# Kernel optimization log

Hardware: AMD Instinct MI355X
Metric: run time of the kernel (lower is better)

## Reference

```python
import jax, jax.numpy as jnp
import numpy as np
import math

D = 256   # d_model / hidden_size
Q = 256   # q_num (query-side nodes)
K = 512   # k_num (key-side nodes)
NEG = -9e15


def _forward(q_enc, k_enc, rel_k, rel_v, k_adj,
             W_glob, b_glob, W_gv0, b_gv0, W_gv1, b_gv1,
             W_gq, b_gq, W_lq, b_lq,
             W_locgate, b_locgate, W_gate, b_gate):
    d = q_enc.shape[-1]
    scale = 1.0 / math.sqrt(d)
    act = jnp.tanh  # activation_func='tanh'

    # --- global sigmoid blending of k_enc with the mean query encoding ---
    q_glob_enc = jnp.mean(q_enc, axis=0)                       # [d]
    k_s = jax.nn.sigmoid((q_glob_enc @ W_glob + b_glob) @ k_enc.T * scale)  # [K]
    k_s = k_s[:, None]                                         # [K,1]
    g_1 = q_glob_enc @ W_gv0 + b_gv0                           # [d]
    k_1 = k_enc @ W_gv1 + b_gv1                                # [K,d]
    k_enc2 = (1.0 - k_s) * k_1 + k_s * g_1                     # [K,d]

    # --- global relation-aware attention over k nodes ---
    q_glob = q_enc @ W_gq + b_gq                               # [Q,d]
    qk_logit = q_glob @ k_enc2.T                               # [Q,K]
    qk_r = jnp.einsum('qd,qkd->qk', q_glob, rel_k)             # [Q,K]
    glob_attn = jax.nn.softmax(act((qk_logit + qk_r) * scale), axis=-1)  # [Q,K]

    # --- local adjacency-masked attention ---
    q_loc = q_enc @ W_lq + b_lq                                # [Q,d]
    qnk_logit = q_loc @ k_enc2.T                               # [Q,K]
    qnk_r = jnp.einsum('qd,qkd->qk', q_loc, rel_k)             # [Q,K]
    loc_attn = act((qnk_logit + qnk_r) * scale)                # [Q,K]
    # loc_weight_rep[q,i,j] = loc_attn[q,j]  (repeat + view in torch)
    mask = (k_adj != 0)[None, :, :]                            # [1,K,K]
    masked = jnp.where(mask, loc_attn[:, None, :], NEG)        # [Q,K,K]
    attn_adj_norm = jax.nn.softmax(masked, axis=-1)            # [Q,K,K]
    k_loc = jnp.einsum('qij,jd->qid', attn_adj_norm, k_enc2)   # [Q,K,d]

    # --- local gate between neighborhood value and self value ---
    # sigmoid(cat([k_loc, k_self]) @ W_locgate + b); k_self is broadcast k_enc2
    Wg1, Wg2 = W_locgate[:d], W_locgate[d:]                    # [d,1] each
    gate_logit = (jnp.einsum('qid,d->qi', k_loc, Wg1[:, 0])
                  + (k_enc2 @ Wg2)[None, :, 0] + b_locgate[0])  # [Q,K]
    loc_gate = jax.nn.sigmoid(gate_logit)[..., None]           # [Q,K,1]
    k_awr = loc_gate * k_loc + (1.0 - loc_gate) * k_enc2[None, :, :]  # [Q,K,d]

    # --- aggregate with global attention + relation values ---
    k_matmul = jnp.einsum('qk,qkd->qd', glob_attn, k_awr)      # [Q,d]
    k_r_matmul = jnp.einsum('qk,qkd->qd', glob_attn, rel_v)    # [Q,d]
    q_enc_new = k_matmul + k_r_matmul                          # [Q,d]

    # --- residual gate ---
    Wq1, Wq2 = W_gate[:d], W_gate[d:]
    gate = jax.nn.sigmoid(q_enc_new @ Wq1 + q_enc @ Wq2 + b_gate)  # [Q,1]
    h = gate * q_enc_new + (1.0 - gate) * q_enc                # [Q,d]
    return h


def setup_inputs() -> dict:
    key = jax.random.key(0)
    ks = jax.random.split(key, 16)
    def w(k, shape):
        return jax.random.normal(k, shape, jnp.float32) * 0.02
    return {
        'q_enc': jax.random.normal(ks[0], (Q, D), jnp.float32),
        'k_enc': jax.random.normal(ks[1], (K, D), jnp.float32),
        'rel_k': jax.random.normal(ks[2], (Q, K, D), jnp.float32) * 0.1,
        'rel_v': jax.random.normal(ks[3], (Q, K, D), jnp.float32) * 0.1,
        'k_adj': jax.random.randint(ks[4], (K, K), 0, 2, jnp.int64) if jax.config.jax_enable_x64 else jax.random.randint(ks[4], (K, K), 0, 2, jnp.int32),
        'W_glob': w(ks[5], (D, D)), 'b_glob': jnp.zeros((D,), jnp.float32),
        'W_gv0': w(ks[6], (D, D)), 'b_gv0': jnp.zeros((D,), jnp.float32),
        'W_gv1': w(ks[7], (D, D)), 'b_gv1': jnp.zeros((D,), jnp.float32),
        'W_gq': w(ks[8], (D, D)), 'b_gq': jnp.zeros((D,), jnp.float32),
        'W_lq': w(ks[9], (D, D)), 'b_lq': jnp.zeros((D,), jnp.float32),
        'W_locgate': w(ks[10], (2 * D, 1)), 'b_locgate': jnp.zeros((1,), jnp.float32),
        'W_gate': w(ks[11], (2 * D, 1)), 'b_gate': jnp.zeros((1,), jnp.float32),
    }


def reference(q_enc, k_enc, rel_k, rel_v, k_adj,
              W_glob, b_glob, W_gv0, b_gv0, W_gv1, b_gv1,
              W_gq, b_gq, W_lq, b_lq,
              W_locgate, b_locgate, W_gate, b_gate):
    return _forward(q_enc, k_enc, rel_k, rel_v, k_adj,
                    W_glob, b_glob, W_gv0, b_gv0, W_gv1, b_gv1,
                    W_gq, b_gq, W_lq, b_lq,
                    W_locgate, b_locgate, W_gate, b_gate)
```

## Files before the change

### kernel.cpp

```cpp
#include <hip/hip_runtime.h>
#include <math.h>

#define QN 256
#define KN 512
#define DN 256
#define SCALE 0.0625f

typedef __attribute__((ext_vector_type(8))) short short8v;
typedef __attribute__((ext_vector_type(4))) float f32x4;

__device__ __forceinline__ float sigf(float x){ return 1.0f/(1.0f+expf(-x)); }

__device__ __forceinline__ unsigned short f2bf(float x){
  unsigned u = __float_as_uint(x);
  unsigned r = (u + 0x7FFFu + ((u >> 16) & 1u)) >> 16;
  return (unsigned short)r;
}

__device__ __forceinline__ short8v ld8(const unsigned short* p){
  ushort4 a = *(const ushort4*)p;
  ushort4 b = *(const ushort4*)(p + 16);
  short8v r;
  r[0]=(short)a.x; r[1]=(short)a.y; r[2]=(short)a.z; r[3]=(short)a.w;
  r[4]=(short)b.x; r[5]=(short)b.y; r[6]=(short)b.z; r[7]=(short)b.w;
  return r;
}

__device__ __forceinline__ float wave_red(float v){
  #pragma unroll
  for (int off = 32; off; off >>= 1) v += __shfl_down(v, off);
  return v;
}

__global__ void kA2(const float* __restrict__ q_enc,
                    const float* __restrict__ W_glob, const float* __restrict__ W_gv0,
                    float* __restrict__ party0, float* __restrict__ party1,
                    const int* __restrict__ kadj, unsigned short* __restrict__ mbf){
  __shared__ float sm[256][9];
  __shared__ float qm[8];
  int b = blockIdx.x, t = threadIdx.x;
  int j0 = b*8;
  #pragma unroll
  for (int i = 0; i < 8; ++i){
    int gi = b*2048 + i*256 + t;
    int4 v = ((const int4*)kadj)[gi];
    ushort4 o;
    o.x = v.x ? 0x3F80 : 0; o.y = v.y ? 0x3F80 : 0;
    o.z = v.z ? 0x3F80 : 0; o.w = v.w ? 0x3F80 : 0;
    ((ushort4*)mbf)[gi] = o;
  }
  float4 lo = *(const float4*)(q_enc + (size_t)t*DN + j0);
  float4 hi = *(const float4*)(q_enc + (size_t)t*DN + j0 + 4);
  sm[t][0]=lo.x; sm[t][1]=lo.y; sm[t][2]=lo.z; sm[t][3]=lo.w;
  sm[t][4]=hi.x; sm[t][5]=hi.y; sm[t][6]=hi.z; sm[t][7]=hi.w;
  __syncthreads();
  #pragma unroll
  for (int s = 128; s > 0; s >>= 1){
    if (t < s){
      #pragma unroll
      for (int j = 0; j < 8; ++j) sm[t][j] += sm[t+s][j];
    }
    __syncthreads();
  }
  if (t < 8) qm[t] = sm[0][t] * (1.0f/QN);
  __syncthreads();
  float a0 = 0.f, a1 = 0.f;
  #pragma unroll
  for (int j = 0; j < 8; ++j){
    float s = qm[j];
    a0 = fmaf(s, W_glob[(size_t)(j0+j)*DN + t], a0);
    a1 = fmaf(s, W_gv0[(size_t)(j0+j)*DN + t], a1);
  }
  party0[b*256 + t] = a0; party1[b*256 + t] = a1;
}

__global__ void k23(const float* __restrict__ k_enc,
                    const float* __restrict__ W_gv1, const float* __restrict__ b_gv1,
                    const float* __restrict__ party0, const float* __restrict__ party1,
                    const float* __restrict__ b_glob, const float* __restrict__ b_gv0,
                    const float* __restrict__ W_locgate,
                    float* __restrict__ k_enc2, float* __restrict__ cvec,
                    float* __restrict__ gl2,
                    const float* __restrict__ q_enc,
                    const float* __restrict__ W_gq, const float* __restrict__ b_gq,
                    const float* __restrict__ W_lq, const float* __restrict__ b_lq,
                    float* __restrict__ q_glob, float* __restrict__ q_loc){
  __shared__ float sh1[256];
  __shared__ float red8[8];
  int bid = blockIdx.x, t = threadIdx.x;
  int w = t >> 6, lane = t & 63;
  if (bid < 512){
    int k = bid;
    float tg = b_glob[t], g1v = b_gv0[t];
    #pragma unroll 8
    for (int b2 = 0; b2 < 32; ++b2){
      tg  += party0[b2*256 + t];
      g1v += party1[b2*256 + t];
    }
    float kv = k_enc[(size_t)k*DN + t];
    sh1[t] = kv;
    float part = wave_red(kv * tg);
    if (lane == 0) red8[w] = part;
    __syncthreads();
    float dot = red8[0] + red8[1] + red8[2] + red8[3];
    float ks = sigf(dot * SCALE);
    float acc = b_gv1[t];
    #pragma unroll 8
    for (int j = 0; j < DN; ++j) acc = fmaf(sh1[j], W_gv1[(size_t)j*DN + t], acc);
    float v = (1.f - ks)*acc + ks*g1v;
    k_enc2[(size_t)k*DN + t] = v;
    float pc = wave_red(v * W_locgate[t]);
    float pg = wave_red(v * W_locgate[DN + t]);
    __syncthreads();
    if (lane == 0){ red8[w] = pc; red8[4 + w] = pg; }
    __syncthreads();
    if (t == 0) cvec[k] = red8[0] + red8[1] + red8[2] + red8[3];
    if (t == 1) gl2[k]  = red8[4] + red8[5] + red8[6] + red8[7];
  } else {
    int q = bid - 512;
    sh1[t] = q_enc[(size_t)q*DN + t];
    __syncthreads();
    float a = b_gq[t], b = b_lq[t];
    #pragma unroll 8
    for (int j = 0; j < DN; ++j){
      float s = sh1[j];
      a = fmaf(s, W_gq[(size_t)j*DN + t], a);
      b = fmaf(s, W_lq[(size_t)j*DN + t], b);
    }
    q_glob[(size_t)q*DN + t] = a; q_loc[(size_t)q*DN + t] = b;
  }
}

__global__ __launch_bounds__(256) void kbf(const float* __restrict__ rel_k,
                    const float* __restrict__ rel_v,
                    const float* __restrict__ q_glob, const float* __restrict__ q_loc,
                    const float* __restrict__ ke2, const float* __restrict__ cvec,
                    float* __restrict__ exs, float* __restrict__ ev,
                    unsigned short* __restrict__ ebf, unsigned short* __restrict__ ecbf,
                    float* __restrict__ part){
  __shared__ f32x4 sacc[4][16][4];
  int t = threadIdx.x;
  int wv = t >> 6, lane = t & 63;
  int g = lane >> 4, l16 = lane & 15;
  int b = blockIdx.x;
  int q = b >> 3, slice = b & 7;
  int base = lane & 48;
  f32x4 racc[4];
  #pragma unroll
  for (int it = 0; it < 4; ++it) racc[it] = (f32x4){0.f,0.f,0.f,0.f};
  #pragma unroll 1
  for (int kq = 0; kq < 4; ++kq){
    int k = slice*64 + kq*16 + wv*4 + g;
    size_t rowoff = ((size_t)q*KN + k)*DN;
    float p1 = 0.f, p2 = 0.f, p3 = 0.f, p4 = 0.f;
    f32x4 y[4];
    #pragma unroll
    for (int it = 0; it < 4; ++it){
      int d = it*64 + l16*4;
      f32x4 x = __builtin_nontemporal_load((const f32x4*)(rel_k + rowoff + d));
      y[it]   = __builtin_nontemporal_load((const f32x4*)(rel_v + rowoff + d));
      float4 a  = *(const float4*)(q_glob + (size_t)q*DN + d);
      float4 bb = *(const float4*)(q_loc  + (size_t)q*DN + d);
      float4 c  = *(const float4*)(ke2    + (size_t)k*DN + d);
      p1 += x[0]*a.x + x[1]*a.y + x[2]*a.z + x[3]*a.w;
      p2 += x[0]*bb.x + x[1]*bb.y + x[2]*bb.z + x[3]*bb.w;
      p3 += c.x*a.x + c.y*a.y + c.z*a.z + c.w*a.w;
      p4 += c.x*bb.x + c.y*bb.y + c.z*bb.z + c.w*bb.w;
    }
    #pragma unroll
    for (int off = 8; off; off >>= 1){
      p1 += __shfl_down(p1, off); p2 += __shfl_down(p2, off);
      p3 += __shfl_down(p3, off); p4 += __shfl_down(p4, off);
    }
    float p13 = __shfl(p1 + p3, base);
    float p24 = __shfl(p2 + p4, base);
    float exv = expf(tanhf(p13*SCALE));
    float evv = expf(tanhf(p24*SCALE));
    if (l16 == 0){
      size_t idx = (size_t)q*KN + k;
      exs[idx] = exv;
      ev[idx] = evv;
      ebf[idx] = f2bf(evv);
      ecbf[idx] = f2bf(evv * cvec[k]);
    }
    #pragma unroll
    for (int it = 0; it < 4; ++it){
      racc[it][0] = fmaf(exv, y[it][0], racc[it][0]);
      racc[it][1] = fmaf(exv, y[it][1], racc[it][1]);
      racc[it][2] = fmaf(exv, y[it][2], racc[it][2]);
      racc[it][3] = fmaf(exv, y[it][3], racc[it][3]);
    }
  }
  #pragma unroll
  for (int h = 16; h <= 32; h <<= 1){
    #pragma unroll
    for (int it = 0; it < 4; ++it){
      racc[it][0] += __shfl_xor(racc[it][0], h);
      racc[it][1] += __shfl_xor(racc[it][1], h);
      racc[it][2] += __shfl_xor(racc[it][2], h);
      racc[it][3] += __shfl_xor(racc[it][3], h);
    }
  }
  if (lane < 16){
    #pragma unroll
    for (int it = 0; it < 4; ++it) sacc[wv][lane][it] = racc[it];
  }
  __syncthreads();
  if (t < 64){
    int it = t >> 4, lb = t & 15;
    f32x4 r0 = sacc[0][lb][it], r1 = sacc[1][lb][it];
    f32x4 r2 = sacc[2][lb][it], r3 = sacc[3][lb][it];
    f32x4 r = r0 + r1 + r2 + r3;
    int d = it*64 + lb*4;
    *(f32x4*)(part + ((size_t)slice*QN + q)*DN + d) = r;
  }
}

__global__ __launch_bounds__(256) void kcA2m(const unsigned short* __restrict__ ebf,
                                             const unsigned short* __restrict__ ecbf,
                                             const unsigned short* __restrict__ mbf,
                                             const float* __restrict__ exs,
                                             const float* __restrict__ gl2,
                                             const float* __restrict__ blg_p,
                                             unsigned short* __restrict__ wvbf,
                                             float* __restrict__ v2){
  __shared__ unsigned short Ae[16*520];
  __shared__ unsigned short Ac[16*520];
  __shared__ unsigned short Bm[64*520];
  int t = threadIdx.x;
  int i0 = blockIdx.x*64, q0 = blockIdx.y*16;
  #pragma unroll
  for (int it = 0; it < 4; ++it){
    int c = t + 256*it; int row = c >> 6, col = (c & 63)*8;
    *(uint4*)&Ae[row*520 + col] = *(const uint4*)&ebf[(size_t)(q0+row)*KN + col];
    *(uint4*)&Ac[row*520 + col] = *(const uint4*)&ecbf[(size_t)(q0+row)*KN + col];
  }
  #pragma unroll
  for (int it = 0; it < 16; ++it){
    int c = t + 256*it; int row = c >> 6, col = (c & 63)*8;
    *(uint4*)&Bm[row*520 + col] = *(const uint4*)&mbf[(size_t)(i0+row)*KN + col];
  }
  __syncthreads();
  int w = t >> 6, l = t & 63;
  int g16 = l >> 4, l16 = l & 15;
  f32x4 aS = {0.f,0.f,0.f,0.f}, aN = {0.f,0.f,0.f,0.f};
  const unsigned short* pe = &Ae[l16*520];
  const unsigned short* pc = &Ac[l16*520];
  const unsigned short* pb = &Bm[(16*w + l16)*520];
  #pragma unroll
  for (int kk = 0; kk < 16; ++kk){
    int k0 = kk*32 + 4*g16;
    short8v fa = ld8(pe + k0);
    short8v fc = ld8(pc + k0);
    short8v fb = ld8(pb + k0);
    aS = __builtin_amdgcn_mfma_f32_16x16x32_bf16(fa, fb, aS, 0, 0, 0);
    aN = __builtin_amdgcn_mfma_f32_16x16x32_bf16(fc, fb, aN, 0, 0, 0);
  }
  float blg = blg_p[0];
  int i = i0 + 16*w + l16;
  float gli = gl2[i];
  #pragma unroll
  for (int r = 0; r < 4; ++r){
    int q = q0 + 4*g16 + r;
    size_t idx = (size_t)q*KN + i;
    float s = aS[r], n = aN[r];
    float lgv = sigf(n/s + gli + blg);
    float ex = exs[idx];
    wvbf[idx] = f2bf(ex*lgv/s);
    v2[idx] = ex*(1.f - lgv);
  }
}

__global__ __launch_bounds__(256) void kcC2m(const unsigned short* __restrict__ wvbf,
                                             const unsigned short* __restrict__ mbf,
                                             const float* __restrict__ ev,
                                             const float* __restrict__ v2,
                                             float* __restrict__ coef){
  __shared__ unsigned short Aw[16*520];
  __shared__ unsigned short Bm2[512*72];
  int t = threadIdx.x;
  int j0 = blockIdx.x*64, q0 = blockIdx.y*16;
  #pragma unroll
  for (int it = 0; it < 4; ++it){
    int c = t + 256*it; int row = c >> 6, col = (c & 63)*8;
    *(uint4*)&Aw[row*520 + col] = *(const uint4*)&wvbf[(size_t)(q0+row)*KN + col];
  }
  #pragma unroll
  for (int it = 0; it < 16; ++it){
    int c = t + 256*it; int row = c >> 3, col = (c & 7)*8;
    *(uint4*)&Bm2[row*72 + col] = *(const uint4*)&mbf[(size_t)row*KN + j0 + col];
  }
  __syncthreads();
  int w = t >> 6, l = t & 63;
  int g16 = l >> 4, l16 = l & 15;
  f32x4 aU = {0.f,0.f,0.f,0.f};
  const unsigned short* pa = &Aw[l16*520];
  int nn = 16*w + l16;
  #pragma unroll
  for (int kk = 0; kk < 16; ++kk){
    int k0 = kk*32 + 4*g16;
    short8v fa = ld8(pa + k0);
    short8v fb;
    #pragma unroll
    for (int e = 0; e < 4; ++e){
      fb[e]   = (short)Bm2[(k0+e)*72 + nn];
      fb[4+e] = (short)Bm2[(k0+16+e)*72 + nn];
    }
    aU = __builtin_amdgcn_mfma_f32_16x16x32_bf16(fa, fb, aU, 0, 0, 0);
  }
  int j = j0 + nn;
  #pragma unroll
  for (int r = 0; r < 4; ++r){
    int q = q0 + 4*g16 + r;
    size_t idx = (size_t)q*KN + j;
    coef[idx] = aU[r]*ev[idx] + v2[idx];
  }
}

__global__ __launch_bounds__(512) void kE2(const float* __restrict__ ke2,
                                           const float* __restrict__ exs,
                                           const float* __restrict__ coef,
                                           const float* __restrict__ part,
                                           const float* __restrict__ q_enc,
                                           const float* __restrict__ W_gate,
                                           const float* __restrict__ b_gate,
                                           float* __restrict__ out){
  __shared__ float red[512];
  __shared__ float4 pacc[8][64];
  int q = blockIdx.x, t = threadIdx.x, w = t >> 6, lane = t & 63;
  red[t] = exs[(size_t)q*KN + t];
  __syncthreads();
  #pragma unroll
  for (int s = 256; s > 0; s >>= 1){
    if (t < s) red[t] += red[t+s];
    __syncthreads();
  }
  float invs = 1.0f / red[0];
  f32x4 pv = *(const f32x4*)(part + ((size_t)w*QN + q)*DN + lane*4);
  float4 acc = make_float4(pv[0], pv[1], pv[2], pv[3]);
  int kbase = w*64;
  #pragma unroll 8
  for (int kk = 0; kk < 64; ++kk){
    int k = kbase + kk;
    float ck = coef[(size_t)q*KN + k];
    float4 kv = ((const float4*)(ke2 + (size_t)k*DN))[lane];
    acc.x = fmaf(ck, kv.x, acc.x);
    acc.y = fmaf(ck, kv.y, acc.y);
    acc.z = fmaf(ck, kv.z, acc.z);
    acc.w = fmaf(ck, kv.w, acc.w);
  }
  pacc[w][lane] = acc;
  __syncthreads();
  if (t < 64){
    float4 r = pacc[0][t];
    #pragma unroll
    for (int w2 = 1; w2 < 8; ++w2){
      float4 p = pacc[w2][t];
      r.x += p.x; r.y += p.y; r.z += p.z; r.w += p.w;
    }
    r.x *= invs; r.y *= invs; r.z *= invs; r.w *= invs;
    float4 qe = ((const float4*)(q_enc + (size_t)q*DN))[t];
    float4 w1 = ((const float4*)(W_gate))[t];
    float4 w2v = ((const float4*)(W_gate + DN))[t];
    float pd = r.x*w1.x + r.y*w1.y + r.z*w1.z + r.w*w1.w
             + qe.x*w2v.x + qe.y*w2v.y + qe.z*w2v.z + qe.w*w2v.w;
    #pragma unroll
    for (int off = 32; off; off >>= 1) pd += __shfl_down(pd, off);
    float gate = sigf(__shfl(pd, 0) + b_gate[0]);
    float4 h;
    h.x = gate*r.x + (1.f-gate)*qe.x;
    h.y = gate*r.y + (1.f-gate)*qe.y;
    h.z = gate*r.z + (1.f-gate)*qe.z;
    h.w = gate*r.w + (1.f-gate)*qe.w;
    ((float4*)(out + (size_t)q*DN))[t] = h;
  }
}

extern "C" void kernel_launch(void* const* d_in, const int* in_sizes, int n_in,
                              void* d_out, int out_size, void* d_ws, size_t ws_size,
                              hipStream_t stream){
  const float* q_enc     = (const float*)d_in[0];
  const float* k_enc     = (const float*)d_in[1];
  const float* rel_k     = (const float*)d_in[2];
  const float* rel_v     = (const float*)d_in[3];
  const int*   k_adj     = (const int*)  d_in[4];
  const float* W_glob    = (const float*)d_in[5];
  const float* b_glob    = (const float*)d_in[6];
  const float* W_gv0     = (const float*)d_in[7];
  const float* b_gv0     = (const float*)d_in[8];
  const float* W_gv1     = (const float*)d_in[9];
  const float* b_gv1     = (const float*)d_in[10];
  const float* W_gq      = (const float*)d_in[11];
  const float* b_gq      = (const float*)d_in[12];
  const float* W_lq      = (const float*)d_in[13];
  const float* b_lq      = (const float*)d_in[14];
  const float* W_locgate = (const float*)d_in[15];
  const float* b_locgate = (const float*)d_in[16];
  const float* W_gate    = (const float*)d_in[17];
  const float* b_gate    = (const float*)d_in[18];
  float* out = (float*)d_out;

  float* ws = (float*)d_ws;
  float* party0   = ws;
  float* party1   = party0 + 8192;
  float* k_enc2   = party1 + 8192;
  float* cvec     = k_enc2 + 131072;
  float* gl2      = cvec + 512;
  float* q_glob   = gl2 + 512;
  float* q_loc    = q_glob + 65536;
  float* exs      = q_loc + 65536;
  float* evb      = exs + 131072;
  float* v2       = evb + 131072;
  float* coef     = v2 + 131072;
  float* part     = coef + 131072;
  unsigned short* mbf  = (unsigned short*)(part + 524288);
  unsigned short* ebf  = mbf + 262144;
  unsigned short* ecbf = ebf + 131072;
  unsigned short* wvbf = ecbf + 131072;

  kA2<<<32, 256, 0, stream>>>(q_enc, W_glob, W_gv0, party0, party1, k_adj, mbf);
  k23<<<768, 256, 0, stream>>>(k_enc, W_gv1, b_gv1, party0, party1, b_glob, b_gv0,
                               W_locgate, k_enc2, cvec, gl2,
                               q_enc, W_gq, b_gq, W_lq, b_lq, q_glob, q_loc);
  kbf<<<2048, 256, 0, stream>>>(rel_k, rel_v, q_glob, q_loc, k_enc2, cvec,
                                exs, evb, ebf, ecbf, part);
  kcA2m<<<dim3(8, 16), 256, 0, stream>>>(ebf, ecbf, mbf, exs, gl2, b_locgate, wvbf, v2);
  kcC2m<<<dim3(8, 16), 256, 0, stream>>>(wvbf, mbf, evb, v2, coef);
  kE2<<<256, 512, 0, stream>>>(k_enc2, exs, coef, part, q_enc, W_gate, b_gate, out);
}
```

Measured before the change: 90.07 us.

## Prefetch rel rows in kbf, drop fp32 ev buffer, widen final kernel

The main streaming kernel now hoists the q_glob/q_loc loads out of its loop and software-prefetches the next rel_k/rel_v rows, keeping more loads in flight. The fp32 ev buffer is removed and kcC2m reconstructs ev from its bf16 copy, which cuts global writes and reads but lowers the precision of that factor. The final kernel moves to 1024 threads, with each wave covering 32 keys instead of 64. The prefetch raises register pressure, which may reduce occupancy.

```diff
diff --git a/kernel.cpp b/kernel.cpp
--- a/kernel.cpp
+++ b/kernel.cpp
@@ -135,7 +135,7 @@
                     const float* __restrict__ rel_v,
                     const float* __restrict__ q_glob, const float* __restrict__ q_loc,
                     const float* __restrict__ ke2, const float* __restrict__ cvec,
-                    float* __restrict__ exs, float* __restrict__ ev,
+                    float* __restrict__ exs,
                     unsigned short* __restrict__ ebf, unsigned short* __restrict__ ecbf,
                     float* __restrict__ part){
   __shared__ f32x4 sacc[4][16][4];
@@ -145,26 +145,47 @@
   int b = blockIdx.x;
   int q = b >> 3, slice = b & 7;
   int base = lane & 48;
+  float4 a4[4], b4[4];
+  #pragma unroll
+  for (int it = 0; it < 4; ++it){
+    int d = it*64 + l16*4;
+    a4[it] = *(const float4*)(q_glob + (size_t)q*DN + d);
+    b4[it] = *(const float4*)(q_loc  + (size_t)q*DN + d);
+  }
   f32x4 racc[4];
   #pragma unroll
   for (int it = 0; it < 4; ++it) racc[it] = (f32x4){0.f,0.f,0.f,0.f};
-  #pragma unroll 1
+
+  int k = slice*64 + wv*4 + g;
+  size_t ro = ((size_t)q*KN + k)*DN;
+  f32x4 x[4], y[4];
+  #pragma unroll
+  for (int it = 0; it < 4; ++it){
+    int d = it*64 + l16*4;
+    x[it] = __builtin_nontemporal_load((const f32x4*)(rel_k + ro + d));
+    y[it] = __builtin_nontemporal_load((const f32x4*)(rel_v + ro + d));
+  }
+  #pragma unroll
   for (int kq = 0; kq < 4; ++kq){
-    int k = slice*64 + kq*16 + wv*4 + g;
-    size_t rowoff = ((size_t)q*KN + k)*DN;
+    f32x4 xn[4], yn[4];
+    if (kq < 3){
+      size_t ro2 = ((size_t)q*KN + (k + 16))*DN;
+      #pragma unroll
+      for (int it = 0; it < 4; ++it){
+        int d = it*64 + l16*4;
+        xn[it] = __builtin_nontemporal_load((const f32x4*)(rel_k + ro2 + d));
+        yn[it] = __builtin_nontemporal_load((const f32x4*)(rel_v + ro2 + d));
+      }
+    }
     float p1 = 0.f, p2 = 0.f, p3 = 0.f, p4 = 0.f;
-    f32x4 y[4];
     #pragma unroll
     for (int it = 0; it < 4; ++it){
       int d = it*64 + l16*4;
-      f32x4 x = __builtin_nontemporal_load((const f32x4*)(rel_k + rowoff + d));
-      y[it]   = __builtin_nontemporal_load((const f32x4*)(rel_v + rowoff + d));
-      float4 a  = *(const float4*)(q_glob + (size_t)q*DN + d);
-      float4 bb = *(const float4*)(q_loc  + (size_t)q*DN + d);
-      float4 c  = *(const float4*)(ke2    + (size_t)k*DN + d);
-      p1 += x[0]*a.x + x[1]*a.y + x[2]*a.z + x[3]*a.w;
-      p2 += x[0]*bb.x + x[1]*bb.y + x[2]*bb.z + x[3]*bb.w;
-      p3 += c.x*a.x + c.y*a.y + c.z*a.z + c.w*a.w;
+      float4 c = *(const float4*)(ke2 + (size_t)k*DN + d);
+      float4 a = a4[it], bb = b4[it];
+      p1 += x[it][0]*a.x  + x[it][1]*a.y  + x[it][2]*a.z  + x[it][3]*a.w;
+      p2 += x[it][0]*bb.x + x[it][1]*bb.y + x[it][2]*bb.z + x[it][3]*bb.w;
+      p3 += c.x*a.x  + c.y*a.y  + c.z*a.z  + c.w*a.w;
       p4 += c.x*bb.x + c.y*bb.y + c.z*bb.z + c.w*bb.w;
     }
     #pragma unroll
@@ -179,7 +200,6 @@
     if (l16 == 0){
       size_t idx = (size_t)q*KN + k;
       exs[idx] = exv;
-      ev[idx] = evv;
       ebf[idx] = f2bf(evv);
       ecbf[idx] = f2bf(evv * cvec[k]);
     }
@@ -189,6 +209,11 @@
       racc[it][1] = fmaf(exv, y[it][1], racc[it][1]);
       racc[it][2] = fmaf(exv, y[it][2], racc[it][2]);
       racc[it][3] = fmaf(exv, y[it][3], racc[it][3]);
+    }
+    if (kq < 3){
+      #pragma unroll
+      for (int it = 0; it < 4; ++it){ x[it] = xn[it]; y[it] = yn[it]; }
+      k += 16;
     }
   }
   #pragma unroll
@@ -273,7 +298,7 @@
 
 __global__ __launch_bounds__(256) void kcC2m(const unsigned short* __restrict__ wvbf,
                                              const unsigned short* __restrict__ mbf,
-                                             const float* __restrict__ ev,
+                                             const unsigned short* __restrict__ ebf,
                                              const float* __restrict__ v2,
                                              float* __restrict__ coef){
   __shared__ unsigned short Aw[16*520];
@@ -313,22 +338,23 @@
   for (int r = 0; r < 4; ++r){
     int q = q0 + 4*g16 + r;
     size_t idx = (size_t)q*KN + j;
-    coef[idx] = aU[r]*ev[idx] + v2[idx];
-  }
-}
-
-__global__ __launch_bounds__(512) void kE2(const float* __restrict__ ke2,
-                                           const float* __restrict__ exs,
-                                           const float* __restrict__ coef,
-                                           const float* __restrict__ part,
-                                           const float* __restrict__ q_enc,
-                                           const float* __restrict__ W_gate,
-                                           const float* __restrict__ b_gate,
-                                           float* __restrict__ out){
+    float evv = __uint_as_float(((unsigned)ebf[idx]) << 16);
+    coef[idx] = aU[r]*evv + v2[idx];
+  }
+}
+
+__global__ __launch_bounds__(1024) void kE2(const float* __restrict__ ke2,
+                                            const float* __restrict__ exs,
+                                            const float* __restrict__ coef,
+                                            const float* __restrict__ part,
+                                            const float* __restrict__ q_enc,
+                                            const float* __restrict__ W_gate,
+                                            const float* __restrict__ b_gate,
+                                            float* __restrict__ out){
   __shared__ float red[512];
-  __shared__ float4 pacc[8][64];
+  __shared__ float4 pacc[16][64];
   int q = blockIdx.x, t = threadIdx.x, w = t >> 6, lane = t & 63;
-  red[t] = exs[(size_t)q*KN + t];
+  if (t < 512) red[t] = exs[(size_t)q*KN + t];
   __syncthreads();
   #pragma unroll
   for (int s = 256; s > 0; s >>= 1){
@@ -336,11 +362,16 @@
     __syncthreads();
   }
   float invs = 1.0f / red[0];
-  f32x4 pv = *(const f32x4*)(part + ((size_t)w*QN + q)*DN + lane*4);
-  float4 acc = make_float4(pv[0], pv[1], pv[2], pv[3]);
-  int kbase = w*64;
+  float4 acc;
+  if ((w & 1) == 0){
+    f32x4 pv = *(const f32x4*)(part + ((size_t)(w >> 1)*QN + q)*DN + lane*4);
+    acc = make_float4(pv[0], pv[1], pv[2], pv[3]);
+  } else {
+    acc = make_float4(0.f, 0.f, 0.f, 0.f);
+  }
+  int kbase = w*32;
   #pragma unroll 8
-  for (int kk = 0; kk < 64; ++kk){
+  for (int kk = 0; kk < 32; ++kk){
     int k = kbase + kk;
     float ck = coef[(size_t)q*KN + k];
     float4 kv = ((const float4*)(ke2 + (size_t)k*DN))[lane];
@@ -354,7 +385,7 @@
   if (t < 64){
     float4 r = pacc[0][t];
     #pragma unroll
-    for (int w2 = 1; w2 < 8; ++w2){
+    for (int w2 = 1; w2 < 16; ++w2){
       float4 p = pacc[w2][t];
       r.x += p.x; r.y += p.y; r.z += p.z; r.w += p.w;
     }
@@ -409,8 +440,7 @@
   float* q_glob   = gl2 + 512;
   float* q_loc    = q_glob + 65536;
   float* exs      = q_loc + 65536;
-  float* evb      = exs + 131072;
-  float* v2       = evb + 131072;
+  float* v2       = exs + 131072;
   float* coef     = v2 + 131072;
   float* part     = coef + 131072;
   unsigned short* mbf  = (unsigned short*)(part + 524288);
@@ -423,8 +453,8 @@
                                W_locgate, k_enc2, cvec, gl2,
                                q_enc, W_gq, b_gq, W_lq, b_lq, q_glob, q_loc);
   kbf<<<2048, 256, 0, stream>>>(rel_k, rel_v, q_glob, q_loc, k_enc2, cvec,
-                                exs, evb, ebf, ecbf, part);
+                                exs, ebf, ecbf, part);
   kcA2m<<<dim3(8, 16), 256, 0, stream>>>(ebf, ecbf, mbf, exs, gl2, b_locgate, wvbf, v2);
-  kcC2m<<<dim3(8, 16), 256, 0, stream>>>(wvbf, mbf, evb, v2, coef);
-  kE2<<<256, 512, 0, stream>>>(k_enc2, exs, coef, part, q_enc, W_gate, b_gate, out);
-}
+  kcC2m<<<dim3(8, 16), 256, 0, stream>>>(wvbf, mbf, ebf, v2, coef);
+  kE2<<<256, 1024, 0, stream>>>(k_enc2, exs, coef, part, q_enc, W_gate, b_gate, out);
+}
```

New measurement: 88.41 us. No clear change (-1.8%).
